# Kernel optimization log

Measured on AMD Instinct MI355X. Metric: run time of the kernel, lower is better.

The kernel has to match this reference:

```python
import jax, jax.numpy as jnp
import numpy as np
from jax import lax

T_NO = 200
SUB_NO = 16
E_NO = 2000
I_NO = 500
T_DATA = 20000
COS_BASIS_NO = 16
COS_SHIFT = 1.0
COS_SCALE = 4.0


def make_cos_basis(T_no):
    # [cos_basis_no, T_no] raised-cosine basis, matches torch loop exactly
    i = jnp.arange(COS_BASIS_NO, dtype=jnp.float32)[:, None]
    phi = (jnp.pi / 2.0) * i
    x = jnp.arange(T_no, dtype=jnp.float32)[None, :]
    raw = COS_SCALE * jnp.log(x + COS_SHIFT)
    basis = 0.5 * jnp.cos(raw - phi) + 0.5
    return jnp.where((raw < phi - jnp.pi) | (raw > phi + jnp.pi), 0.0, basis)


@jax.custom_vjp
def step(x):
    # torch.heaviside(x, 0): 1 for x>0, 0 for x<=0
    return jnp.where(x > 0, 1.0, 0.0).astype(x.dtype)

def _step_fwd(x):
    return step(x), x

def _step_bwd(x, g):
    return (g / (1.0 + jnp.abs(x)) ** 2,)

step.defvjp(_step_fwd, _step_bwd)


def _depthwise_causal(pad, kern_flipped):
    # pad: [T_data+T_no, sub], kern_flipped: [sub, T_no] (already flipped, torch-style)
    lhs = pad.T[None]                      # [1, sub, L]
    rhs = kern_flipped[:, None, :]          # [sub, 1, T_no]
    out = lax.conv_general_dilated(lhs, rhs, (1,), 'VALID',
                                   dimension_numbers=('NCH', 'OIH', 'NCH'),
                                   feature_group_count=SUB_NO)
    return out[0].T                         # [T_data+1, sub]


def _srm_forward(S_e, S_i, C_den, C_syn_e, C_syn_i, Tau_syn_e, Tau_syn_i,
                 W_syn_e, W_syn_i, Delta_syn_e, Delta_syn_i, Tau_spk, W_spk,
                 W_hist, Theta):
    T_no = T_NO
    cos_basis = make_cos_basis(T_no)
    syn_e = S_e @ C_syn_e.T                 # [T_data, sub]
    syn_i = S_i @ C_syn_i.T

    t = jnp.arange(T_no, dtype=jnp.float32)[None, :]
    t_e = jnp.maximum(t - jnp.exp(Delta_syn_e)[:, None], 0.0)
    t_i = jnp.maximum(t - jnp.exp(Delta_syn_i)[:, None], 0.0)
    tt_e = t_e / jnp.exp(Tau_syn_e)[:, None]
    tt_i = t_i / jnp.exp(Tau_syn_i)[:, None]
    e_kern = tt_e * jnp.exp(-tt_e) * jnp.exp(W_syn_e)[:, None]       # [sub, T_no]
    i_kern = -tt_i * jnp.exp(-tt_i) * jnp.exp(W_syn_i)[:, None]

    zpad = jnp.zeros((T_no, SUB_NO), syn_e.dtype)
    filt_e = _depthwise_causal(jnp.concatenate([zpad, syn_e], 0), jnp.flip(e_kern, 1))[:-1]
    filt_i = _depthwise_causal(jnp.concatenate([zpad, syn_i], 0), jnp.flip(i_kern, 1))[:-1]
    syn = filt_e + filt_i                   # [T_data, sub]

    tt_spk = t / jnp.exp(Tau_spk)[:, None]
    spk_kern = tt_spk * jnp.exp(-tt_spk) * jnp.exp(W_spk)[:, None]   # [sub, T_no]
    hist_kern = W_hist @ cos_basis                                    # [sub, T_no]
    spk_kern_f = jnp.flip(spk_kern, 1)
    hist_kern_f = jnp.flip(hist_kern, 1)

    def step_fn(buf, syn_t):
        # buf: [T_no, sub] rolling spike history, buf[-1] = most recent
        hist_in = jnp.einsum('ts,st->s', buf, hist_kern_f)
        spk_in_raw = jnp.einsum('ts,st->s', buf, spk_kern_f)
        spk_in = C_den @ spk_in_raw
        sub_in = hist_in + spk_in + syn_t + Theta
        s = step(sub_in)
        return jnp.concatenate([buf[1:], s[None]], 0), s

    buf0 = jnp.zeros((T_no, SUB_NO), syn.dtype)
    _, spk_out = lax.scan(step_fn, buf0, syn)   # [T_data, sub]

    out_filters = jnp.vstack([e_kern, i_kern, spk_kern, hist_kern])  # [4*sub, T_no]
    return spk_out, out_filters


def setup_inputs() -> dict:
    key = jax.random.key(0)
    ks = jax.random.split(key, 10)
    # sparse-ish spike trains
    S_e = (jax.random.uniform(ks[0], (T_DATA, E_NO)) < 0.02).astype(jnp.float32)
    S_i = (jax.random.uniform(ks[1], (T_DATA, I_NO)) < 0.02).astype(jnp.float32)
    # each synapse maps to exactly one subunit
    C_syn_e = jax.nn.one_hot(jax.random.randint(ks[2], (E_NO,), 0, SUB_NO), SUB_NO).T.astype(jnp.float32)
    C_syn_i = jax.nn.one_hot(jax.random.randint(ks[3], (I_NO,), 0, SUB_NO), SUB_NO).T.astype(jnp.float32)
    C_den = (jax.random.uniform(ks[4], (SUB_NO, SUB_NO)) < 0.15).astype(jnp.float32)
    ones = jnp.ones(SUB_NO, jnp.float32)
    return {
        'S_e': S_e, 'S_i': S_i, 'C_den': C_den, 'C_syn_e': C_syn_e, 'C_syn_i': C_syn_i,
        'Tau_syn_e': ones * 1.0, 'Tau_syn_i': ones * 1.0,
        'W_syn_e': ones * 0.5, 'W_syn_i': ones * 0.5,
        'Delta_syn_e': ones * 1.0, 'Delta_syn_i': ones * 1.0,
        'Tau_spk': ones * 1.0, 'W_spk': ones * -1.0,
        'W_hist': 0.1 * jax.random.normal(ks[5], (SUB_NO, COS_BASIS_NO), jnp.float32),
        'Theta': -0.5 * ones + 0.1 * jax.random.normal(ks[6], (SUB_NO,), jnp.float32),
    }


def reference(S_e, S_i, C_den, C_syn_e, C_syn_i, Tau_syn_e, Tau_syn_i, W_syn_e,
              W_syn_i, Delta_syn_e, Delta_syn_i, Tau_spk, W_spk, W_hist, Theta):
    return _srm_forward(S_e, S_i, C_den, C_syn_e, C_syn_i, Tau_syn_e, Tau_syn_i,
                        W_syn_e, W_syn_i, Delta_syn_e, Delta_syn_i, Tau_spk, W_spk,
                        W_hist, Theta)
```

## Files before the change

kernel.cpp:

```cpp
#include <hip/hip_runtime.h>

#ifndef M_PI
#define M_PI 3.14159265358979323846
#endif

#define T_DATA 20000
#define E_NO_C 2000
#define I_NO_C 500
#define SUB 16
#define TNO 200
#define NGRP 5000
#define NSUP 2500

typedef float v2f __attribute__((ext_vector_type(2)));

template <bool B> struct BC { static constexpr bool v = B; };

__device__ __forceinline__ float quad_sum(float v) {
  int a = __builtin_amdgcn_mov_dpp(__float_as_int(v), 177, 0xf, 0xf, true);
  v += __int_as_float(a);
  int b = __builtin_amdgcn_mov_dpp(__float_as_int(v), 78, 0xf, 0xf, true);
  v += __int_as_float(b);
  return v;
}

__device__ __forceinline__ void bar_drain() {
  asm volatile("s_waitcnt lgkmcnt(0)" ::: "memory");
  __builtin_amdgcn_s_barrier();
  asm volatile("" ::: "memory");
}
__device__ __forceinline__ void bar_raw() {
  asm volatile("" ::: "memory");
  __builtin_amdgcn_s_barrier();
  asm volatile("" ::: "memory");
}

__global__ void filters_k(const float* __restrict__ Tau_e, const float* __restrict__ Tau_i,
                          const float* __restrict__ W_e,  const float* __restrict__ W_i,
                          const float* __restrict__ D_e,  const float* __restrict__ D_i,
                          const float* __restrict__ Tau_spk, const float* __restrict__ W_spk,
                          const float* __restrict__ W_hist,
                          float* __restrict__ filt_out) {
  int id = blockIdx.x * blockDim.x + threadIdx.x;
  if (id >= 64 * TNO) return;
  int r = id / TNO, x = id % TNO;
  int s = r & 15, kind = r >> 4;
  double xd = (double)x;
  double val;
  if (kind == 0) {
    double te = xd - exp((double)D_e[s]); te = te > 0.0 ? te : 0.0;
    double tt = te / exp((double)Tau_e[s]);
    val = tt * exp(-tt) * exp((double)W_e[s]);
  } else if (kind == 1) {
    double ti = xd - exp((double)D_i[s]); ti = ti > 0.0 ? ti : 0.0;
    double tt = ti / exp((double)Tau_i[s]);
    val = -tt * exp(-tt) * exp((double)W_i[s]);
  } else if (kind == 2) {
    double tt = xd / exp((double)Tau_spk[s]);
    val = tt * exp(-tt) * exp((double)W_spk[s]);
  } else {
    double raw = 4.0 * log(xd + 1.0);
    double acc = 0.0;
    for (int i = 0; i < 16; ++i) {
      double phi = (M_PI / 2.0) * (double)i;
      double b = (raw < phi - M_PI || raw > phi + M_PI) ? 0.0
                                                        : (0.5 * cos(raw - phi) + 0.5);
      acc += (double)W_hist[s * 16 + i] * b;
    }
    val = acc;
  }
  filt_out[id] = (float)val;
}

#define ETILE 500
__global__ __launch_bounds__(256) void synmm_k(const float* __restrict__ S,
                                               const float* __restrict__ C,
                                               float* __restrict__ out, int E) {
  __shared__ __align__(16) float Cs[16][ETILE];
  int tid = threadIdx.x;
  int s = tid & 15, tt = tid >> 4;
  long t = (long)blockIdx.x * 16 + tt;
  const float* Srow = S + t * E;
  float acc = 0.f;
  for (int tb = 0; tb < E; tb += ETILE) {
    __syncthreads();
    for (int i = tid; i < 16 * ETILE; i += 256) {
      int s2 = i / ETILE, k2 = i - s2 * ETILE;
      Cs[s2][k2] = C[(long)s2 * E + tb + k2];
    }
    __syncthreads();
    const float* Crow = &Cs[s][0];
    const float* Sp = Srow + tb;
#pragma unroll 2
    for (int e = 0; e < ETILE; e += 4) {
      float4 a = *(const float4*)(Sp + e);
      float4 c = *(const float4*)(Crow + e);
      acc = fmaf(a.x, c.x, acc); acc = fmaf(a.y, c.y, acc);
      acc = fmaf(a.z, c.z, acc); acc = fmaf(a.w, c.w, acc);
    }
  }
  out[t * 16 + s] = acc;
}

__global__ void conv_k(const float* __restrict__ syn_e, const float* __restrict__ syn_i,
                       const float* __restrict__ filt, const float* __restrict__ Theta,
                       float* __restrict__ synTh) {
  __shared__ float ek[16][201];
  __shared__ float ik[16][201];
  int tid = threadIdx.x;
  for (int idx = tid; idx < 16 * TNO; idx += 256) {
    ek[idx / TNO][idx % TNO] = filt[idx];
    ik[idx / TNO][idx % TNO] = filt[16 * TNO + idx];
  }
  __syncthreads();
  int s = tid & 15, tt = tid >> 4;
  int t = blockIdx.x * 16 + tt;
  float acc = Theta[s];
  if (t >= TNO) {
#pragma unroll 4
    for (int j = 0; j < TNO; ++j) {
      int u = t - 1 - j;
      acc += ek[s][j] * syn_e[u * 16 + s] + ik[s][j] * syn_i[u * 16 + s];
    }
  } else {
    for (int j = 0; j < t; ++j) {
      int u = t - 1 - j;
      acc += ek[s][j] * syn_e[u * 16 + s] + ik[s][j] * syn_i[u * 16 + s];
    }
  }
  synTh[t * 16 + s] = acc;
}

__global__ __launch_bounds__(512, 1) void scan16_k(const float* __restrict__ synTh,
                                                   const float* __restrict__ filt,
                                                   const float* __restrict__ C_den,
                                                   const float* __restrict__ Tau_spk,
                                                   const float* __restrict__ W_spk,
                                                   float* __restrict__ spk_out) {
  __shared__ __align__(16) float ring[16][452];
  __shared__ __align__(16) float oPartF[2][5][64][2];
  __shared__ __align__(16) float farsumF[2][2][64];
  __shared__ __align__(16) float synStage[2][4][16][20];
  const int tid = threadIdx.x;
  const int widx = tid >> 6;
  const int l = tid & 63;
  const int s = l & 15, q = l >> 4;

  for (int i = tid; i < 16 * 452; i += 512) (&ring[0][0])[i] = 0.f;
  for (int i = tid; i < 2 * 5 * 64 * 2; i += 512) (&oPartF[0][0][0][0])[i] = 0.f;
  for (int i = tid; i < 2 * 2 * 64; i += 512) (&farsumF[0][0][0])[i] = 0.f;
  __syncthreads();
  if (widx == 7) {
    int e0 = 4 * l;
    float4 v = *(const float4*)&synTh[e0];
    int t0 = e0 >> 4, s0 = e0 & 15;
    int g = t0 >> 2, K = t0 & 3;
    synStage[0][g & 3][s0 + 0][K] = v.x;
    synStage[0][g & 3][s0 + 1][K] = v.y;
    synStage[0][g & 3][s0 + 2][K] = v.z;
    synStage[0][g & 3][s0 + 3][K] = v.w;
  }
  __syncthreads();

  if (widx == 0) {
    const float* hrow = filt + (48 + s) * TNO;
    float hk[15];
#pragma unroll
    for (int i = 0; i < 15; ++i) hk[i] = hrow[i];

    float t0v = Tau_spk[0], w0v = W_spk[0];
    bool okrow = (Tau_spk[s] == t0v) && (W_spk[s] == w0v);
    unsigned cd = 0u;
#pragma unroll
    for (int j = 0; j < 16; ++j) {
      float cv = C_den[s * 16 + j];
      okrow = okrow && (cv == 0.f || cv == 1.f);
      cd |= (cv != 0.f) ? (1u << j) : 0u;
    }
    const bool uni = (bool)__all((int)okrow);

    const double tau  = exp((double)Tau_spk[s]);
    const double aa   = exp(-1.0 / tau);
    const double c2a  = exp((double)W_spk[s]) * aa / tau;
    const double twoa = 2.0 * aa;
    const double na2  = -aa * aa;

    double twoa4[4], na24[4], c2a4[4], yd0a[4], yd1a[4];
    float cden4[4];
#pragma unroll
    for (int r = 0; r < 4; ++r) {
      int j = 4 * q + r;
      double tj = exp((double)Tau_spk[j]);
      double aj = exp(-1.0 / tj);
      twoa4[r] = 2.0 * aj; na24[r] = -aj * aj;
      c2a4[r]  = exp((double)W_spk[j]) * aj / tj;
      yd0a[r] = 0.0; yd1a[r] = 0.0;
      cden4[r] = C_den[s * 16 + j];
    }

    double zA = 0.0, zB = 0.0;
    float mixu = 0.f, mix1 = 0.f;
    float sgPrev = 0.f;
    float S0 = 0.f, S1 = 0.f, S2 = 0.f, S3 = 0.f;

    float ocA0, ocA1, ocA2, ocA3;
    float uB0, uB1, uB2, uB3;
    float sB0, sB1, sB2, sB3;
    float ccBk0, ccBk1, ccBk2, ccBk3;
    {
      float4 fsA_r = *(const float4*)&farsumF[0][0][4 * s];
      float4 fsB_r = *(const float4*)&farsumF[0][1][4 * s];
      float4 synA_r = *(const float4*)&synStage[0][0][s][0];
      float4 synB_r = *(const float4*)&synStage[0][1][s][0];
      float z0 = 0.f;
      ocA0 = ((z0 + fsA_r.x) + (synA_r.x + z0)) + z0;
      ocA1 = ((z0 + fsA_r.y) + (synA_r.y + z0)) + z0;
      ocA2 = ((z0 + fsA_r.z) + (synA_r.z + z0)) + z0;
      ocA3 = ((z0 + fsA_r.w) + (synA_r.w + z0)) + z0;
      uB0 = z0 + fsB_r.x; uB1 = z0 + fsB_r.y; uB2 = z0 + fsB_r.z; uB3 = z0 + fsB_r.w;
      sB0 = synB_r.x; sB1 = synB_r.y; sB2 = synB_r.z; sB3 = synB_r.w;
      ccBk0 = z0; ccBk1 = z0; ccBk2 = z0; ccBk3 = z0;
    }

#define STEP(SGD, PRE, SGOUT)                                                 \
    {                                                                         \
      float sub = fmaf(hk[0], (SGD), (PRE));                                  \
      unsigned long long bal = __ballot(sub > 0.f);                           \
      float sg = sub > 0.f ? 1.f : 0.f;                                       \
      if constexpr (UNI) {                                                    \
        unsigned xm = (unsigned)bal & cd;              \
        double zc = fma(twoa, zB, fma(na2, zA, c2a * (double)__popc(xm)));    \
        zA = zB; zB = zc;                                                     \
        mixu = (float)zA;                                                     \
      } else {                                                                \
        unsigned mk = (unsigned)bal & 0xFFFFu;                                \
        float p = 0.f;                                                        \
        _Pragma("unroll")                                                     \
        for (int r = 0; r < 4; ++r) {                                         \
          double xr = (double)((mk >> (4 * q + r)) & 1u);                     \
          double y2 = fma(twoa4[r], yd1a[r], fma(na24[r], yd0a[r], c2a4[r] * xr)); \
          yd0a[r] = yd1a[r]; yd1a[r] = y2;                                    \
          p = fmaf(cden4[r], (float)y2, p);                                   \
        }                                                                     \
        p += __shfl_xor(p, 16); p += __shfl_xor(p, 32);                       \
        float mixn = mix1; mix1 = p;                                          \
        mixu = mixn;                                                          \
      }                                                                       \
      (SGOUT) = sg;                                                           \
    }

    auto scan_loop = [&](auto uc) {
      constexpr bool UNI = decltype(uc)::v;
      for (int M = 0; M < NSUP; ++M) {
        float SA0, SA1, SA2, SA3;
        STEP(sgPrev, ocA0 + mixu, SA0)
        float pend2 = hk[1] * SA0;
        float pend3 = hk[2] * SA0;
        STEP(SA0, ocA1 + mixu, SA1)
        pend3 = fmaf(hk[1], SA1, pend3);
        STEP(SA1, (ocA2 + mixu) + pend2, SA2)
        STEP(SA2, (ocA3 + mixu) + pend3, SA3)

        if (l < 16) {
          int u = (8 * M) & 255;
          float4 w0; w0.x = SA0; w0.y = SA1; w0.z = SA2; w0.w = SA3;
          *(float4*)&ring[s][u] = w0;
          if (u < 192) *(float4*)&ring[s][u + 256] = w0;
        }

        float cB0 = fmaf(hk[1], SA2, fmaf(hk[2], SA1, hk[3] * SA0));
        float cB1 = fmaf(hk[1], SA3, fmaf(hk[2], SA2, fmaf(hk[3], SA1, hk[4] * SA0)));
        float cB2 = fmaf(hk[2], SA3, fmaf(hk[3], SA2, fmaf(hk[4], SA1, hk[5] * SA0)));
        float cB3 = fmaf(hk[3], SA3, fmaf(hk[4], SA2, fmaf(hk[5], SA1, hk[6] * SA0)));
        float ocB0 = (uB0 + (sB0 + cB0)) + ccBk0;
        float ocB1 = (uB1 + (sB1 + cB1)) + ccBk1;
        float ocB2 = (uB2 + (sB2 + cB2)) + ccBk2;
        float ocB3 = (uB3 + (sB3 + cB3)) + ccBk3;

        float SB0, SB1, SB2, SB3;
        STEP(SA3, ocB0 + mixu, SB0)
        float pend2b = hk[1] * SB0;
        float pend3b = hk[2] * SB0;
        STEP(SB0, ocB1 + mixu, SB1)
        pend3b = fmaf(hk[1], SB1, pend3b);
        STEP(SB1, (ocB2 + mixu) + pend2b, SB2)
        STEP(SB2, (ocB3 + mixu) + pend3b, SB3)

        if (l < 16) {
          int u = (8 * M + 4) & 255;
          float4 w0; w0.x = SB0; w0.y = SB1; w0.z = SB2; w0.w = SB3;
          *(float4*)&ring[s][u] = w0;
          if (u < 192) *(float4*)&ring[s][u + 256] = w0;
        }

        bar_raw();

        const int Mn = M + 1;
        const int gAn = 2 * Mn, gBn = 2 * Mn + 1;
        float4 fsA_r = *(const float4*)&farsumF[Mn & 1][0][4 * s];
        float4 fsB_r = *(const float4*)&farsumF[Mn & 1][1][4 * s];
        float4 synA_r = *(const float4*)&synStage[(gAn >> 2) & 1][gAn & 3][s][0];
        float4 synB_r = *(const float4*)&synStage[(gBn >> 2) & 1][gBn & 3][s][0];

        float cA0 = fmaf(hk[1], SB2, fmaf(hk[2], SB1, hk[3] * SB0));
        float cA1 = fmaf(hk[1], SB3, fmaf(hk[2], SB2, fmaf(hk[3], SB1, hk[4] * SB0)));
        float cA2 = fmaf(hk[2], SB3, fmaf(hk[3], SB2, fmaf(hk[4], SB1, hk[5] * SB0)));
        float cA3 = fmaf(hk[3], SB3, fmaf(hk[4], SB2, fmaf(hk[5], SB1, hk[6] * SB0)));
        float ccA0 = fmaf(hk[7], SA0, fmaf(hk[6], SA1, fmaf(hk[5], SA2, hk[4] * SA3)));
        float ccA1 = fmaf(hk[8], SA0, fmaf(hk[7], SA1, fmaf(hk[6], SA2, hk[5] * SA3)));
        float ccA2 = fmaf(hk[9], SA0, fmaf(hk[8], SA1, fmaf(hk[7], SA2, hk[6] * SA3)));
        float ccA3 = fmaf(hk[10], SA0, fmaf(hk[9], SA1, fmaf(hk[8], SA2, hk[7] * SA3)));
        float nrA0 = fmaf(hk[11], S0, fmaf(hk[10], S1, fmaf(hk[9], S2, hk[8] * S3)));
        float nrA1 = fmaf(hk[12], S0, fmaf(hk[11], S1, fmaf(hk[10], S2, hk[9] * S3)));
        float nrA2 = fmaf(hk[13], S0, fmaf(hk[12], S1, fmaf(hk[11], S2, hk[10] * S3)));
        float nrA3 = fmaf(hk[14], S0, fmaf(hk[13], S1, fmaf(hk[12], S2, hk[11] * S3)));
        float ccB0 = fmaf(hk[7], SB0, fmaf(hk[6], SB1, fmaf(hk[5], SB2, hk[4] * SB3)));
        float ccB1 = fmaf(hk[8], SB0, fmaf(hk[7], SB1, fmaf(hk[6], SB2, hk[5] * SB3)));
        float ccB2 = fmaf(hk[9], SB0, fmaf(hk[8], SB1, fmaf(hk[7], SB2, hk[6] * SB3)));
        float ccB3 = fmaf(hk[10], SB0, fmaf(hk[9], SB1, fmaf(hk[8], SB2, hk[7] * SB3)));
        float nrB0 = fmaf(hk[11], SA0, fmaf(hk[10], SA1, fmaf(hk[9], SA2, hk[8] * SA3)));
        float nrB1 = fmaf(hk[12], SA0, fmaf(hk[11], SA1, fmaf(hk[10], SA2, hk[9] * SA3)));
        float nrB2 = fmaf(hk[13], SA0, fmaf(hk[12], SA1, fmaf(hk[11], SA2, hk[10] * SA3)));
        float nrB3 = fmaf(hk[14], SA0, fmaf(hk[13], SA1, fmaf(hk[12], SA2, hk[11] * SA3)));

        ocA0 = ((nrA0 + fsA_r.x) + (synA_r.x + cA0)) + ccA0;
        ocA1 = ((nrA1 + fsA_r.y) + (synA_r.y + cA1)) + ccA1;
        ocA2 = ((nrA2 + fsA_r.z) + (synA_r.z + cA2)) + ccA2;
        ocA3 = ((nrA3 + fsA_r.w) + (synA_r.w + cA3)) + ccA3;
        uB0 = nrB0 + fsB_r.x; uB1 = nrB1 + fsB_r.y;
        uB2 = nrB2 + fsB_r.z; uB3 = nrB3 + fsB_r.w;
        sB0 = synB_r.x; sB1 = synB_r.y; sB2 = synB_r.z; sB3 = synB_r.w;
        ccBk0 = ccB0; ccBk1 = ccB1; ccBk2 = ccB2; ccBk3 = ccB3;

        S0 = SB0; S1 = SB1; S2 = SB2; S3 = SB3;
        sgPrev = SB3;
        bar_drain();
      }
    };
    if (uni) scan_loop(BC<true>{});
    else     scan_loop(BC<false>{});
#undef STEP
  } else if (widx == 4) {
    for (int M = 0; M < NSUP; ++M) {
      bar_raw();
      bar_raw();
    }
  } else if (widx == 7) {
    const int s2 = l >> 2, K = l & 3;
    const float* hrow = filt + (48 + s2) * TNO;
    float hc5[32];
#pragma unroll
    for (int x = 0; x < 32; ++x) hc5[x] = hrow[12 + K + x];

    for (int M = 0; M < NSUP; ++M) {
      float4 vv;
      const bool doStage = (M & 1) && (2 * M + 2 < NGRP);
      if (doStage) vv = *(const float4*)&synTh[(2 * M + 2) * 64 + 4 * l];

      int pos0 = (8 * M - 36) & 255;
      const float4* rp = (const float4*)&ring[s2][pos0];
      float e[36];
#pragma unroll
      for (int i = 0; i < 9; ++i) {
        float4 R = rp[i];
        e[4 * i + 0] = R.x; e[4 * i + 1] = R.y; e[4 * i + 2] = R.z; e[4 * i + 3] = R.w;
      }
      float f5v[2];
#pragma unroll
      for (int p = 0; p < 2; ++p) {
        float oo[4];
#pragma unroll
        for (int c = 0; c < 4; ++c) {
          v2f p01, p23, p45, p67, PR7, PR5, PR3, PR1;
          int ofs = 4 * p + 8 * c;
          p01.x = e[ofs + 0]; p01.y = e[ofs + 1];
          p23.x = e[ofs + 2]; p23.y = e[ofs + 3];
          p45.x = e[ofs + 4]; p45.y = e[ofs + 5];
          p67.x = e[ofs + 6]; p67.y = e[ofs + 7];
          PR7.x = hc5[31 - 8 * c]; PR7.y = hc5[30 - 8 * c];
          PR5.x = hc5[29 - 8 * c]; PR5.y = hc5[28 - 8 * c];
          PR3.x = hc5[27 - 8 * c]; PR3.y = hc5[26 - 8 * c];
          PR1.x = hc5[25 - 8 * c]; PR1.y = hc5[24 - 8 * c];
          v2f a = PR7 * p01; a += PR5 * p23; a += PR3 * p45; a += PR1 * p67;
          oo[c] = a.x + a.y;
        }
        f5v[p] = (oo[0] + oo[1]) + (oo[2] + oo[3]);
      }

      const int slot = M & 1, wbuf = (M + 1) & 1;
      float2 pa = *(const float2*)&oPartF[slot][0][l][0];
      float2 pb = *(const float2*)&oPartF[slot][1][l][0];
      float2 pc = *(const float2*)&oPartF[slot][2][l][0];
      float2 pd = *(const float2*)&oPartF[slot][3][l][0];
      float2 pe = *(const float2*)&oPartF[slot][4][l][0];
      float t0e = pa.x + pb.x;
      float t1e = pc.x + pd.x;
      float t2e = pe.x + f5v[0];
      farsumF[wbuf][0][l] = (t0e + t1e) + t2e;
      float t0o = pa.y + pb.y;
      float t1o = pc.y + pd.y;
      float t2o = pe.y + f5v[1];
      farsumF[wbuf][1][l] = (t0o + t1o) + t2o;

      if (doStage) {
        int e0 = (2 * M + 2) * 64 + 4 * l;
        int t0i = e0 >> 4, s0 = e0 & 15;
        int g = t0i >> 2, Kk = t0i & 3;
        int buf = (g >> 2) & 1;
        synStage[buf][g & 3][s0 + 0][Kk] = vv.x;
        synStage[buf][g & 3][s0 + 1][Kk] = vv.y;
        synStage[buf][g & 3][s0 + 2][Kk] = vv.z;
        synStage[buf][g & 3][s0 + 3][Kk] = vv.w;
      }

      bar_drain();

      if ((M & 3) == 0 && M > 0) {
        int n = 2 * M;
        int We = (4 * n - 1) & 255;
        if (We < 191) We += 256;
        int base2 = We - 31;
#pragma unroll
        for (int r = 0; r < 2; ++r) {
          int eo = 64 * (n - 8) + 256 * r + 4 * l;
          int t0i = eo >> 4, s0 = eo & 15;
          int pos = base2 + (t0i - 4 * (n - 8));
          float4 w;
          w.x = ring[s0 + 0][pos]; w.y = ring[s0 + 1][pos];
          w.z = ring[s0 + 2][pos]; w.w = ring[s0 + 3][pos];
          *(float4*)&spk_out[eo] = w;
        }
      }
      bar_drain();
    }
    {
      int n = NGRP;
      int We = (4 * n - 1) & 255;
      if (We < 191) We += 256;
      int base2 = We - 31;
#pragma unroll
      for (int r = 0; r < 2; ++r) {
        int eo = 64 * (n - 8) + 256 * r + 4 * l;
        int t0i = eo >> 4, s0 = eo & 15;
        int pos = base2 + (t0i - 4 * (n - 8));
        float4 w;
        w.x = ring[s0 + 0][pos]; w.y = ring[s0 + 1][pos];
        w.z = ring[s0 + 2][pos]; w.w = ring[s0 + 3][pos];
        *(float4*)&spk_out[eo] = w;
      }
    }
  } else {
    const int f = (widx < 4) ? (widx - 1) : (widx - 2);
    const int s2 = l >> 2, qq = l & 3;
    const float* hrow = filt + (48 + s2) * TNO;
    const int base = 196 - 32 * f - 8 * qq;
    float ca[11];
#pragma unroll
    for (int m = 0; m < 11; ++m) {
      int hidx = base + m;
      ca[m] = (hidx <= 199) ? hrow[hidx] : 0.f;
    }
    v2f pr[11];
    pr[0].x = 0.f; pr[0].y = 0.f;
#pragma unroll
    for (int m = 1; m < 11; ++m) { pr[m].x = ca[m]; pr[m].y = ca[m - 1]; }

    for (int M = 0; M < NSUP; ++M) {
      int W0 = (8 * M - 188 + 32 * f + 8 * qq) & 255;
      const float4* rp = (const float4*)&ring[s2][W0];
      float4 V0 = rp[0], V1 = rp[1], V2 = rp[2];
      v2f p01, p23, p45, p67, q01, q23, q45, q67;
      p01.x = V0.x; p01.y = V0.y; p23.x = V0.z; p23.y = V0.w;
      p45.x = V1.x; p45.y = V1.y; p67.x = V1.z; p67.y = V1.w;
      q01.x = V1.x; q01.y = V1.y; q23.x = V1.z; q23.y = V1.w;
      q45.x = V2.x; q45.y = V2.y; q67.x = V2.z; q67.y = V2.w;
      float o0, o1, o2, o3, o4, o5, o6, o7;
      { v2f a = pr[7] * p01;  a += pr[5] * p23; a += pr[3] * p45; a += pr[1] * p67; o0 = a.x + a.y; }
      { v2f a = pr[8] * p01;  a += pr[6] * p23; a += pr[4] * p45; a += pr[2] * p67; o1 = a.x + a.y; }
      { v2f a = pr[9] * p01;  a += pr[7] * p23; a += pr[5] * p45; a += pr[3] * p67; o2 = a.x + a.y; }
      { v2f a = pr[10] * p01; a += pr[8] * p23; a += pr[6] * p45; a += pr[4] * p67; o3 = a.x + a.y; }
      { v2f a = pr[7] * q01;  a += pr[5] * q23; a += pr[3] * q45; a += pr[1] * q67; o4 = a.x + a.y; }
      { v2f a = pr[8] * q01;  a += pr[6] * q23; a += pr[4] * q45; a += pr[2] * q67; o5 = a.x + a.y; }
      { v2f a = pr[9] * q01;  a += pr[7] * q23; a += pr[5] * q45; a += pr[3] * q67; o6 = a.x + a.y; }
      { v2f a = pr[10] * q01; a += pr[8] * q23; a += pr[6] * q45; a += pr[4] * q67; o7 = a.x + a.y; }
      o0 = quad_sum(o0); o1 = quad_sum(o1); o2 = quad_sum(o2); o3 = quad_sum(o3);
      o4 = quad_sum(o4); o5 = quad_sum(o5); o6 = quad_sum(o6); o7 = quad_sum(o7);
      float myoE = (qq == 0) ? o0 : (qq == 1) ? o1 : (qq == 2) ? o2 : o3;
      float myoO = (qq == 0) ? o4 : (qq == 1) ? o5 : (qq == 2) ? o6 : o7;
      const int slot = (M + 1) & 1;
      float2 w2; w2.x = myoE; w2.y = myoO;
      *(float2*)&oPartF[slot][f][l][0] = w2;
      bar_raw();
      bar_drain();
    }
  }
}

extern "C" void kernel_launch(void* const* d_in, const int* in_sizes, int n_in,
                              void* d_out, int out_size, void* d_ws, size_t ws_size,
                              hipStream_t stream) {
  const float* S_e     = (const float*)d_in[0];
  const float* S_i     = (const float*)d_in[1];
  const float* C_den   = (const float*)d_in[2];
  const float* C_syn_e = (const float*)d_in[3];
  const float* C_syn_i = (const float*)d_in[4];
  const float* Tau_e   = (const float*)d_in[5];
  const float* Tau_i   = (const float*)d_in[6];
  const float* W_e     = (const float*)d_in[7];
  const float* W_i     = (const float*)d_in[8];
  const float* D_e     = (const float*)d_in[9];
  const float* D_i     = (const float*)d_in[10];
  const float* Tau_spk = (const float*)d_in[11];
  const float* W_spk   = (const float*)d_in[12];
  const float* W_hist  = (const float*)d_in[13];
  const float* Theta   = (const float*)d_in[14];

  float* out     = (float*)d_out;
  float* spk_out = out;
  float* filt    = out + 320000;

  float* ws    = (float*)d_ws;
  float* syn_e = ws;
  float* syn_i = ws + 320000;
  float* synTh = ws + 640000;

  filters_k<<<50, 256, 0, stream>>>(Tau_e, Tau_i, W_e, W_i, D_e, D_i,
                                    Tau_spk, W_spk, W_hist, filt);
  synmm_k<<<1250, 256, 0, stream>>>(S_e, C_syn_e, syn_e, E_NO_C);
  synmm_k<<<1250, 256, 0, stream>>>(S_i, C_syn_i, syn_i, I_NO_C);
  conv_k<<<1250, 256, 0, stream>>>(syn_e, syn_i, filt, Theta, synTh);
  scan16_k<<<1, 512, 0, stream>>>(synTh, filt, C_den, Tau_spk, W_spk, spk_out);
}
```

Before: 1.868 ms.

## Fold far-history partial sum into scan wave and drop one barrier per step

The wave that merged the far-history partial sums (and staged synTh) goes away. The scan wave now keeps a 36-entry register history of recent spikes and computes the fifth convolution partial itself, gathering the other partials with shuffles. Staging moves to wave 4, and the block shrinks from 512 to 448 threads with one barrier per super-step instead of two. This trims barrier latency on the serial critical path, at the cost of more register pressure and extra arithmetic in the latency-bound scan wave.

```diff
diff --git a/kernel.cpp b/kernel.cpp
--- a/kernel.cpp
+++ b/kernel.cpp
@@ -26,11 +26,6 @@
 
 __device__ __forceinline__ void bar_drain() {
   asm volatile("s_waitcnt lgkmcnt(0)" ::: "memory");
-  __builtin_amdgcn_s_barrier();
-  asm volatile("" ::: "memory");
-}
-__device__ __forceinline__ void bar_raw() {
-  asm volatile("" ::: "memory");
   __builtin_amdgcn_s_barrier();
   asm volatile("" ::: "memory");
 }
@@ -131,7 +126,7 @@
   synTh[t * 16 + s] = acc;
 }
 
-__global__ __launch_bounds__(512, 1) void scan16_k(const float* __restrict__ synTh,
+__global__ __launch_bounds__(448, 1) void scan17_k(const float* __restrict__ synTh,
                                                    const float* __restrict__ filt,
                                                    const float* __restrict__ C_den,
                                                    const float* __restrict__ Tau_spk,
@@ -139,18 +134,16 @@
                                                    float* __restrict__ spk_out) {
   __shared__ __align__(16) float ring[16][452];
   __shared__ __align__(16) float oPartF[2][5][64][2];
-  __shared__ __align__(16) float farsumF[2][2][64];
   __shared__ __align__(16) float synStage[2][4][16][20];
   const int tid = threadIdx.x;
   const int widx = tid >> 6;
   const int l = tid & 63;
   const int s = l & 15, q = l >> 4;
 
-  for (int i = tid; i < 16 * 452; i += 512) (&ring[0][0])[i] = 0.f;
-  for (int i = tid; i < 2 * 5 * 64 * 2; i += 512) (&oPartF[0][0][0][0])[i] = 0.f;
-  for (int i = tid; i < 2 * 2 * 64; i += 512) (&farsumF[0][0][0])[i] = 0.f;
+  for (int i = tid; i < 16 * 452; i += 448) (&ring[0][0])[i] = 0.f;
+  for (int i = tid; i < 2 * 5 * 64 * 2; i += 448) (&oPartF[0][0][0][0])[i] = 0.f;
   __syncthreads();
-  if (widx == 7) {
+  if (widx == 4) {
     int e0 = 4 * l;
     float4 v = *(const float4*)&synTh[e0];
     int t0 = e0 >> 4, s0 = e0 & 15;
@@ -167,6 +160,9 @@
     float hk[15];
 #pragma unroll
     for (int i = 0; i < 15; ++i) hk[i] = hrow[i];
+    float hc5[32];
+#pragma unroll
+    for (int x = 0; x < 32; ++x) hc5[x] = hrow[12 + q + x];
 
     float t0v = Tau_spk[0], w0v = W_spk[0];
     bool okrow = (Tau_spk[s] == t0v) && (W_spk[s] == w0v);
@@ -202,22 +198,23 @@
     float mixu = 0.f, mix1 = 0.f;
     float sgPrev = 0.f;
     float S0 = 0.f, S1 = 0.f, S2 = 0.f, S3 = 0.f;
+    float hist[36];
+#pragma unroll
+    for (int i = 0; i < 36; ++i) hist[i] = 0.f;
 
     float ocA0, ocA1, ocA2, ocA3;
     float uB0, uB1, uB2, uB3;
     float sB0, sB1, sB2, sB3;
     float ccBk0, ccBk1, ccBk2, ccBk3;
     {
-      float4 fsA_r = *(const float4*)&farsumF[0][0][4 * s];
-      float4 fsB_r = *(const float4*)&farsumF[0][1][4 * s];
       float4 synA_r = *(const float4*)&synStage[0][0][s][0];
       float4 synB_r = *(const float4*)&synStage[0][1][s][0];
       float z0 = 0.f;
-      ocA0 = ((z0 + fsA_r.x) + (synA_r.x + z0)) + z0;
-      ocA1 = ((z0 + fsA_r.y) + (synA_r.y + z0)) + z0;
-      ocA2 = ((z0 + fsA_r.z) + (synA_r.z + z0)) + z0;
-      ocA3 = ((z0 + fsA_r.w) + (synA_r.w + z0)) + z0;
-      uB0 = z0 + fsB_r.x; uB1 = z0 + fsB_r.y; uB2 = z0 + fsB_r.z; uB3 = z0 + fsB_r.w;
+      ocA0 = ((z0 + z0) + (synA_r.x + z0)) + z0;
+      ocA1 = ((z0 + z0) + (synA_r.y + z0)) + z0;
+      ocA2 = ((z0 + z0) + (synA_r.z + z0)) + z0;
+      ocA3 = ((z0 + z0) + (synA_r.w + z0)) + z0;
+      uB0 = z0; uB1 = z0; uB2 = z0; uB3 = z0;
       sB0 = synB_r.x; sB1 = synB_r.y; sB2 = synB_r.z; sB3 = synB_r.w;
       ccBk0 = z0; ccBk1 = z0; ccBk2 = z0; ccBk3 = z0;
     }
@@ -252,6 +249,48 @@
     auto scan_loop = [&](auto uc) {
       constexpr bool UNI = decltype(uc)::v;
       for (int M = 0; M < NSUP; ++M) {
+        const int idx = (s << 2) | q;
+        float2 oP0 = *(const float2*)&oPartF[M & 1][0][idx][0];
+        float2 oP1 = *(const float2*)&oPartF[M & 1][1][idx][0];
+        float2 oP2 = *(const float2*)&oPartF[M & 1][2][idx][0];
+        float2 oP3 = *(const float2*)&oPartF[M & 1][3][idx][0];
+        float2 oP4 = *(const float2*)&oPartF[M & 1][4][idx][0];
+        const int gAn = 2 * M + 2, gBn = 2 * M + 3;
+        float4 synA_r = *(const float4*)&synStage[(gAn >> 2) & 1][gAn & 3][s][0];
+        float4 synB_r = *(const float4*)&synStage[(gBn >> 2) & 1][gBn & 3][s][0];
+
+        float f5v[2];
+#pragma unroll
+        for (int p = 0; p < 2; ++p) {
+          float oo[4];
+#pragma unroll
+          for (int c = 0; c < 4; ++c) {
+            v2f p01, p23, p45, p67, PR7, PR5, PR3, PR1;
+            int ofs = 4 * p + 8 * c;
+            p01.x = hist[ofs + 0]; p01.y = hist[ofs + 1];
+            p23.x = hist[ofs + 2]; p23.y = hist[ofs + 3];
+            p45.x = hist[ofs + 4]; p45.y = hist[ofs + 5];
+            p67.x = hist[ofs + 6]; p67.y = hist[ofs + 7];
+            PR7.x = hc5[31 - 8 * c]; PR7.y = hc5[30 - 8 * c];
+            PR5.x = hc5[29 - 8 * c]; PR5.y = hc5[28 - 8 * c];
+            PR3.x = hc5[27 - 8 * c]; PR3.y = hc5[26 - 8 * c];
+            PR1.x = hc5[25 - 8 * c]; PR1.y = hc5[24 - 8 * c];
+            v2f a = PR7 * p01; a += PR5 * p23; a += PR3 * p45; a += PR1 * p67;
+            oo[c] = a.x + a.y;
+          }
+          f5v[p] = (oo[0] + oo[1]) + (oo[2] + oo[3]);
+        }
+        float fsEm = ((oP0.x + oP1.x) + (oP2.x + oP3.x)) + (oP4.x + f5v[0]);
+        float fsOm = ((oP0.y + oP1.y) + (oP2.y + oP3.y)) + (oP4.y + f5v[1]);
+        float fsA0 = __shfl(fsEm, s);
+        float fsA1 = __shfl(fsEm, s + 16);
+        float fsA2 = __shfl(fsEm, s + 32);
+        float fsA3 = __shfl(fsEm, s + 48);
+        float fsB0 = __shfl(fsOm, s);
+        float fsB1 = __shfl(fsOm, s + 16);
+        float fsB2 = __shfl(fsOm, s + 32);
+        float fsB3 = __shfl(fsOm, s + 48);
+
         float SA0, SA1, SA2, SA3;
         STEP(sgPrev, ocA0 + mixu, SA0)
         float pend2 = hk[1] * SA0;
@@ -293,14 +332,10 @@
           if (u < 192) *(float4*)&ring[s][u + 256] = w0;
         }
 
-        bar_raw();
-
-        const int Mn = M + 1;
-        const int gAn = 2 * Mn, gBn = 2 * Mn + 1;
-        float4 fsA_r = *(const float4*)&farsumF[Mn & 1][0][4 * s];
-        float4 fsB_r = *(const float4*)&farsumF[Mn & 1][1][4 * s];
-        float4 synA_r = *(const float4*)&synStage[(gAn >> 2) & 1][gAn & 3][s][0];
-        float4 synB_r = *(const float4*)&synStage[(gBn >> 2) & 1][gBn & 3][s][0];
+#pragma unroll
+        for (int i = 0; i < 28; ++i) hist[i] = hist[i + 8];
+        hist[28] = SA0; hist[29] = SA1; hist[30] = SA2; hist[31] = SA3;
+        hist[32] = SB0; hist[33] = SB1; hist[34] = SB2; hist[35] = SB3;
 
         float cA0 = fmaf(hk[1], SB2, fmaf(hk[2], SB1, hk[3] * SB0));
         float cA1 = fmaf(hk[1], SB3, fmaf(hk[2], SB2, fmaf(hk[3], SB1, hk[4] * SB0)));
@@ -323,12 +358,12 @@
         float nrB2 = fmaf(hk[13], SA0, fmaf(hk[12], SA1, fmaf(hk[11], SA2, hk[10] * SA3)));
         float nrB3 = fmaf(hk[14], SA0, fmaf(hk[13], SA1, fmaf(hk[12], SA2, hk[11] * SA3)));
 
-        ocA0 = ((nrA0 + fsA_r.x) + (synA_r.x + cA0)) + ccA0;
-        ocA1 = ((nrA1 + fsA_r.y) + (synA_r.y + cA1)) + ccA1;
-        ocA2 = ((nrA2 + fsA_r.z) + (synA_r.z + cA2)) + ccA2;
-        ocA3 = ((nrA3 + fsA_r.w) + (synA_r.w + cA3)) + ccA3;
-        uB0 = nrB0 + fsB_r.x; uB1 = nrB1 + fsB_r.y;
-        uB2 = nrB2 + fsB_r.z; uB3 = nrB3 + fsB_r.w;
+        ocA0 = ((nrA0 + fsA0) + (synA_r.x + cA0)) + ccA0;
+        ocA1 = ((nrA1 + fsA1) + (synA_r.y + cA1)) + ccA1;
+        ocA2 = ((nrA2 + fsA2) + (synA_r.z + cA2)) + ccA2;
+        ocA3 = ((nrA3 + fsA3) + (synA_r.w + cA3)) + ccA3;
+        uB0 = nrB0 + fsB0; uB1 = nrB1 + fsB1;
+        uB2 = nrB2 + fsB2; uB3 = nrB3 + fsB3;
         sB0 = synB_r.x; sB1 = synB_r.y; sB2 = synB_r.z; sB3 = synB_r.w;
         ccBk0 = ccB0; ccBk1 = ccB1; ccBk2 = ccB2; ccBk3 = ccB3;
 
@@ -342,79 +377,20 @@
 #undef STEP
   } else if (widx == 4) {
     for (int M = 0; M < NSUP; ++M) {
-      bar_raw();
-      bar_raw();
-    }
-  } else if (widx == 7) {
-    const int s2 = l >> 2, K = l & 3;
-    const float* hrow = filt + (48 + s2) * TNO;
-    float hc5[32];
-#pragma unroll
-    for (int x = 0; x < 32; ++x) hc5[x] = hrow[12 + K + x];
-
-    for (int M = 0; M < NSUP; ++M) {
-      float4 vv;
-      const bool doStage = (M & 1) && (2 * M + 2 < NGRP);
-      if (doStage) vv = *(const float4*)&synTh[(2 * M + 2) * 64 + 4 * l];
-
-      int pos0 = (8 * M - 36) & 255;
-      const float4* rp = (const float4*)&ring[s2][pos0];
-      float e[36];
-#pragma unroll
-      for (int i = 0; i < 9; ++i) {
-        float4 R = rp[i];
-        e[4 * i + 0] = R.x; e[4 * i + 1] = R.y; e[4 * i + 2] = R.z; e[4 * i + 3] = R.w;
+      if ((M & 1) == 0) {
+        int g0 = 2 * M + 4;
+        if (g0 < NGRP) {
+          int e0 = g0 * 64 + 4 * l;
+          float4 vv = *(const float4*)&synTh[e0];
+          int t0i = e0 >> 4, s0 = e0 & 15;
+          int g = t0i >> 2, Kk = t0i & 3;
+          int buf = (g >> 2) & 1;
+          synStage[buf][g & 3][s0 + 0][Kk] = vv.x;
+          synStage[buf][g & 3][s0 + 1][Kk] = vv.y;
+          synStage[buf][g & 3][s0 + 2][Kk] = vv.z;
+          synStage[buf][g & 3][s0 + 3][Kk] = vv.w;
+        }
       }
-      float f5v[2];
-#pragma unroll
-      for (int p = 0; p < 2; ++p) {
-        float oo[4];
-#pragma unroll
-        for (int c = 0; c < 4; ++c) {
-          v2f p01, p23, p45, p67, PR7, PR5, PR3, PR1;
-          int ofs = 4 * p + 8 * c;
-          p01.x = e[ofs + 0]; p01.y = e[ofs + 1];
-          p23.x = e[ofs + 2]; p23.y = e[ofs + 3];
-          p45.x = e[ofs + 4]; p45.y = e[ofs + 5];
-          p67.x = e[ofs + 6]; p67.y = e[ofs + 7];
-          PR7.x = hc5[31 - 8 * c]; PR7.y = hc5[30 - 8 * c];
-          PR5.x = hc5[29 - 8 * c]; PR5.y = hc5[28 - 8 * c];
-          PR3.x = hc5[27 - 8 * c]; PR3.y = hc5[26 - 8 * c];
-          PR1.x = hc5[25 - 8 * c]; PR1.y = hc5[24 - 8 * c];
-          v2f a = PR7 * p01; a += PR5 * p23; a += PR3 * p45; a += PR1 * p67;
-          oo[c] = a.x + a.y;
-        }
-        f5v[p] = (oo[0] + oo[1]) + (oo[2] + oo[3]);
-      }
-
-      const int slot = M & 1, wbuf = (M + 1) & 1;
-      float2 pa = *(const float2*)&oPartF[slot][0][l][0];
-      float2 pb = *(const float2*)&oPartF[slot][1][l][0];
-      float2 pc = *(const float2*)&oPartF[slot][2][l][0];
-      float2 pd = *(const float2*)&oPartF[slot][3][l][0];
-      float2 pe = *(const float2*)&oPartF[slot][4][l][0];
-      float t0e = pa.x + pb.x;
-      float t1e = pc.x + pd.x;
-      float t2e = pe.x + f5v[0];
-      farsumF[wbuf][0][l] = (t0e + t1e) + t2e;
-      float t0o = pa.y + pb.y;
-      float t1o = pc.y + pd.y;
-      float t2o = pe.y + f5v[1];
-      farsumF[wbuf][1][l] = (t0o + t1o) + t2o;
-
-      if (doStage) {
-        int e0 = (2 * M + 2) * 64 + 4 * l;
-        int t0i = e0 >> 4, s0 = e0 & 15;
-        int g = t0i >> 2, Kk = t0i & 3;
-        int buf = (g >> 2) & 1;
-        synStage[buf][g & 3][s0 + 0][Kk] = vv.x;
-        synStage[buf][g & 3][s0 + 1][Kk] = vv.y;
-        synStage[buf][g & 3][s0 + 2][Kk] = vv.z;
-        synStage[buf][g & 3][s0 + 3][Kk] = vv.w;
-      }
-
-      bar_drain();
-
       if ((M & 3) == 0 && M > 0) {
         int n = 2 * M;
         int We = (4 * n - 1) & 255;
@@ -490,7 +466,6 @@
       const int slot = (M + 1) & 1;
       float2 w2; w2.x = myoE; w2.y = myoO;
       *(float2*)&oPartF[slot][f][l][0] = w2;
-      bar_raw();
       bar_drain();
     }
   }
@@ -529,5 +504,5 @@
   synmm_k<<<1250, 256, 0, stream>>>(S_e, C_syn_e, syn_e, E_NO_C);
   synmm_k<<<1250, 256, 0, stream>>>(S_i, C_syn_i, syn_i, I_NO_C);
   conv_k<<<1250, 256, 0, stream>>>(syn_e, syn_i, filt, Theta, synTh);
-  scan16_k<<<1, 512, 0, stream>>>(synTh, filt, C_den, Tau_spk, W_spk, spk_out);
-}
+  scan17_k<<<1, 448, 0, stream>>>(synTh, filt, C_den, Tau_spk, W_spk, spk_out);
+}
```

After: 2.240 ms. 19.9% more time.
